# Kernel optimization log

Hardware: AMD Instinct MI355X
Metric: run time of the kernel (lower is better)

## Reference

```python
import jax, jax.numpy as jnp
import numpy as np

KNOTS = 17
T_MAX = 3.0


def _trapezoid(knots=KNOTS, t_max=T_MAX):
    t = jnp.linspace(0.0, t_max, knots, dtype=jnp.float32)
    dt = t_max / (knots - 1)
    w = jnp.full((knots,), 2.0 * dt, dtype=jnp.float32)
    w = w.at[0].set(dt).at[-1].set(dt)
    weights = w * jnp.exp(-t * t / 2.0)
    return t, weights


def setup_inputs() -> dict:
    key = jax.random.key(0)
    k1, k2 = jax.random.split(key)
    z = jax.random.normal(k1, (32, 128, 512), dtype=jnp.float32)   # (T, B, D)
    A = jax.random.normal(k2, (512, 1024), dtype=jnp.float32)      # (D, M) raw, normalized inside
    return {"z": z, "A": A}


def reference(z, A):
    t, weights = _trapezoid()                       # (K,), (K,)
    # column-normalize random projections (matches A / A.norm(dim=0).clamp_min(1e-12))
    norm = jnp.sqrt(jnp.sum(A * A, axis=0, keepdims=True))
    An = A / jnp.maximum(norm, 1e-12)
    proj = jnp.einsum('tbd,dm->tbm', z, An)         # (T, B, M)
    xt = proj[..., None] * t                        # (T, B, M, K) — dominant intermediate
    cos_mean = jnp.mean(jnp.cos(xt), axis=1)        # reduce over B -> (T, M, K)
    sin_mean = jnp.mean(jnp.sin(xt), axis=1)
    target = jnp.exp(-t * t / 2.0)                  # (K,)
    err = (cos_mean - target) ** 2 + sin_mean ** 2  # (T, M, K)
    statistic = err @ weights                       # (T, M)
    statistic = statistic * z.shape[1]              # multiply by B (proj.size(-2))
    return jnp.mean(statistic)
```

## Files before the change

### kernel.cpp

```cpp
#include <hip/hip_runtime.h>
#include <hip/hip_bf16.h>
#include <math.h>

#define T_DIM 32
#define B_DIM 128
#define D_DIM 512
#define M_DIM 1024

constexpr float DT = 0.1875f;
constexpr float INV_2PI = 0.15915494309189535f;

typedef __attribute__((ext_vector_type(8))) short bf16x8;
typedef __attribute__((ext_vector_type(4))) float f32x4;
typedef __attribute__((ext_vector_type(2))) float f32x2;

__device__ __forceinline__ ushort f2bf(float f) {
    unsigned u = __float_as_uint(f);
    u += 0x7FFFu + ((u >> 16) & 1u);
    return (ushort)(u >> 16);
}

__device__ __forceinline__ void gload16(const void* g, void* l) {
    __builtin_amdgcn_global_load_lds(
        (const __attribute__((address_space(1))) void*)g,
        (__attribute__((address_space(3))) void*)l, 16, 0, 0);
}

__device__ __forceinline__ void fast_sincos(float theta, float& s, float& c) {
    float r = theta * INV_2PI;
    r -= floorf(r);
    s = __builtin_amdgcn_sinf(r);
    c = __builtin_amdgcn_cosf(r);
}

__global__ __launch_bounds__(256) void prep_kernel(const float* __restrict__ A,
                                                   const float* __restrict__ z,
                                                   ushort* __restrict__ zb,
                                                   ushort* __restrict__ ant) {
    const int bid = blockIdx.x;
    const int tid = threadIdx.x;

    if (bid >= 64) {
        const size_t base = (size_t)(bid - 64) * 4096 + tid * 8;
#pragma unroll
        for (int j = 0; j < 2; ++j) {
            const size_t i = base + j * 2048;
            const float4 a = *reinterpret_cast<const float4*>(&z[i]);
            const float4 b = *reinterpret_cast<const float4*>(&z[i + 4]);
            uint4 p;
            p.x = (unsigned)f2bf(a.x) | ((unsigned)f2bf(a.y) << 16);
            p.y = (unsigned)f2bf(a.z) | ((unsigned)f2bf(a.w) << 16);
            p.z = (unsigned)f2bf(b.x) | ((unsigned)f2bf(b.y) << 16);
            p.w = (unsigned)f2bf(b.z) | ((unsigned)f2bf(b.w) << 16);
            *reinterpret_cast<uint4*>(&zb[i]) = p;
        }
        return;
    }

    __shared__ float red[256];
    __shared__ float inv[16];
    __shared__ float tile[128][17];

    const int mB = bid * 16;
    const int mo = tid & 15;
    const int dg = tid >> 4;
    float ss = 0.0f;
#pragma unroll 4
    for (int i = 0; i < 32; ++i) {
        const float v = A[(size_t)(dg * 32 + i) * M_DIM + mB + mo];
        ss = fmaf(v, v, ss);
    }
    red[tid] = ss;
    __syncthreads();
    for (int s = 128; s >= 16; s >>= 1) {
        if (tid < s) red[tid] += red[tid + s];
        __syncthreads();
    }
    if (tid < 16) inv[tid] = 1.0f / fmaxf(sqrtf(red[tid]), 1e-12f);

#pragma unroll
    for (int ch = 0; ch < 4; ++ch) {
        const int dB = ch * 128;
#pragma unroll
        for (int q = 0; q < 2; ++q) {
            const int s  = tid + 256 * q;
            const int r  = s >> 2;
            const int c4 = (s & 3) * 4;
            const float4 v = *reinterpret_cast<const float4*>(
                &A[(size_t)(dB + r) * M_DIM + mB + c4]);
            tile[r][c4]     = v.x;
            tile[r][c4 + 1] = v.y;
            tile[r][c4 + 2] = v.z;
            tile[r][c4 + 3] = v.w;
        }
        __syncthreads();
        {
            const int m  = tid >> 4;
            const int d8 = (tid & 15) * 8;
            const float sc = inv[m];
            uint4 p;
            p.x = (unsigned)f2bf(tile[d8 + 0][m] * sc) | ((unsigned)f2bf(tile[d8 + 1][m] * sc) << 16);
            p.y = (unsigned)f2bf(tile[d8 + 2][m] * sc) | ((unsigned)f2bf(tile[d8 + 3][m] * sc) << 16);
            p.z = (unsigned)f2bf(tile[d8 + 4][m] * sc) | ((unsigned)f2bf(tile[d8 + 5][m] * sc) << 16);
            p.w = (unsigned)f2bf(tile[d8 + 6][m] * sc) | ((unsigned)f2bf(tile[d8 + 7][m] * sc) << 16);
            *reinterpret_cast<uint4*>(&ant[(size_t)(mB + m) * D_DIM + dB + d8]) = p;
        }
        __syncthreads();
    }
}

#define CHEB(CS) { const f32x2 nxt = c2 * cur - prev; prev = cur; cur = nxt; CS += cur; }
#define CF_ALL(V) { \
    float s1, c1; fast_sincos((V) * DT, s1, c1); \
    const float c2 = 2.0f * c1; \
    f32x2 prev = {1.0f, 0.0f}; \
    f32x2 cur  = {c1, s1}; \
    cs0 += cur; \
    CHEB(cs1)  CHEB(cs2)  CHEB(cs3)  CHEB(cs4)  CHEB(cs5) \
    CHEB(cs6)  CHEB(cs7)  CHEB(cs8)  CHEB(cs9)  CHEB(cs10) \
    CHEB(cs11) CHEB(cs12) CHEB(cs13) CHEB(cs14) CHEB(cs15) }
#define RED(CS) { \
    CS.x += __shfl_xor(CS.x, 16); CS.x += __shfl_xor(CS.x, 32); \
    CS.y += __shfl_xor(CS.y, 16); CS.y += __shfl_xor(CS.y, 32); }
#define ST(CS, K) { wred[wc][l15][K] = CS.x; wred[wc][l15][16 + K] = CS.y; }
#define FIN(CS, KK) { \
    constexpr float tk = DT * (float)(KK); \
    const float g  = __expf(-0.5f * tk * tk); \
    const float w  = (((KK) == 16) ? DT : 2.0f * DT) * g; \
    const float totC = wred[wc][l15][(KK) - 1]      + CS.x; \
    const float totS = wred[wc][l15][16 + (KK) - 1] + CS.y; \
    const float cm = fmaf(totC, invB, -g); \
    const float sm = totS * invB; \
    s = fmaf(w, fmaf(cm, cm, sm * sm), s); }

__global__ __launch_bounds__(512) void fused_kernel(const ushort* __restrict__ zb,
                                                    const ushort* __restrict__ ant,
                                                    float* __restrict__ partials) {
    __shared__ __align__(16) union SharedU {
        ushort As[128 * 128];
        struct { float wred[4][16][33]; float bred[4]; } r;
    } u;
    __shared__ __align__(16) ushort Bs[64 * 128];

    const int tid  = threadIdx.x;
    const int bid  = blockIdx.x;
    const int idx  = bid >> 3;
    const int t    = (bid & 7) * 4 + (idx & 3);
    const int mBi  = idx >> 2;
    const int mB   = mBi * 64;

    const int wave = tid >> 6;
    const int lane = tid & 63;
    const int wr   = wave >> 2;
    const int wc   = wave & 3;
    const int l15  = lane & 15;
    const int lhi  = lane >> 4;

    const int rofs = lane >> 4;
    const int gl   = lane & 15;

    const ushort* zrow = zb + (size_t)t * B_DIM * D_DIM;

    f32x4 acc[4];
#pragma unroll
    for (int fm = 0; fm < 4; ++fm) acc[fm] = (f32x4)(0.0f);

#pragma unroll
    for (int it = 0; it < 4; ++it) {
        const int k0 = it * 128;
#pragma unroll
        for (int j = 0; j < 4; ++j) {
            const int r0  = wave * 16 + j * 4;
            const int row = r0 + rofs;
            const int gs  = gl ^ (row & 15);
            gload16(&zrow[(size_t)row * D_DIM + k0 + gs * 8], &u.As[r0 * 128]);
        }
#pragma unroll
        for (int j = 0; j < 2; ++j) {
            const int r0  = wave * 8 + j * 4;
            const int row = r0 + rofs;
            const int gs  = gl ^ (row & 15);
            gload16(&ant[(size_t)(mB + row) * D_DIM + k0 + gs * 8], &Bs[r0 * 128]);
        }
        __syncthreads();

#pragma unroll
        for (int ks = 0; ks < 4; ++ks) {
            const int gd = (ks * 4 + lhi) ^ l15;
            const int co = gd * 8;
            const bf16x8 bfrag = *reinterpret_cast<const bf16x8*>(&Bs[(wc * 16 + l15) * 128 + co]);
#pragma unroll
            for (int fm = 0; fm < 4; ++fm) {
                const bf16x8 afrag = *reinterpret_cast<const bf16x8*>(&u.As[(wr * 64 + fm * 16 + l15) * 128 + co]);
                acc[fm] = __builtin_amdgcn_mfma_f32_16x16x32_bf16(afrag, bfrag, acc[fm], 0, 0, 0);
            }
        }
        __syncthreads();
    }

    float (&wred)[4][16][33] = u.r.wred;
    float (&bred)[4] = u.r.bred;

    f32x2 cs0  = {0.f, 0.f}, cs1  = {0.f, 0.f}, cs2  = {0.f, 0.f}, cs3  = {0.f, 0.f};
    f32x2 cs4  = {0.f, 0.f}, cs5  = {0.f, 0.f}, cs6  = {0.f, 0.f}, cs7  = {0.f, 0.f};
    f32x2 cs8  = {0.f, 0.f}, cs9  = {0.f, 0.f}, cs10 = {0.f, 0.f}, cs11 = {0.f, 0.f};
    f32x2 cs12 = {0.f, 0.f}, cs13 = {0.f, 0.f}, cs14 = {0.f, 0.f}, cs15 = {0.f, 0.f};

#pragma unroll
    for (int fm = 0; fm < 4; ++fm) {
        const f32x4 av = acc[fm];
        CF_ALL(av.x) CF_ALL(av.y) CF_ALL(av.z) CF_ALL(av.w)
    }

    RED(cs0)  RED(cs1)  RED(cs2)  RED(cs3)  RED(cs4)  RED(cs5)  RED(cs6)  RED(cs7)
    RED(cs8)  RED(cs9)  RED(cs10) RED(cs11) RED(cs12) RED(cs13) RED(cs14) RED(cs15)

    if (wr == 0 && lane < 16) {
        ST(cs0, 0)   ST(cs1, 1)   ST(cs2, 2)   ST(cs3, 3)
        ST(cs4, 4)   ST(cs5, 5)   ST(cs6, 6)   ST(cs7, 7)
        ST(cs8, 8)   ST(cs9, 9)   ST(cs10, 10) ST(cs11, 11)
        ST(cs12, 12) ST(cs13, 13) ST(cs14, 14) ST(cs15, 15)
    }
    __syncthreads();

    float s = 0.0f;
    if (wr == 1) {
        const float invB = 1.0f / 128.0f;
        FIN(cs0, 1)   FIN(cs1, 2)   FIN(cs2, 3)   FIN(cs3, 4)
        FIN(cs4, 5)   FIN(cs5, 6)   FIN(cs6, 7)   FIN(cs7, 8)
        FIN(cs8, 9)   FIN(cs9, 10)  FIN(cs10, 11) FIN(cs11, 12)
        FIN(cs12, 13) FIN(cs13, 14) FIN(cs14, 15) FIN(cs15, 16)
#pragma unroll
        for (int m = 1; m < 64; m <<= 1) s += __shfl_xor(s, m);
        if (lane == 0) bred[wc] = s;
    }
    __syncthreads();
    if (tid == 0)
        partials[t * 16 + mBi] = bred[0] + bred[1] + bred[2] + bred[3];
}

__global__ __launch_bounds__(256) void finalize_kernel(const float* __restrict__ partials,
                                                       float* __restrict__ out) {
    __shared__ float red[256];
    const int tid = threadIdx.x;
    red[tid] = partials[tid] + partials[tid + 256];
    __syncthreads();
    for (int s = 128; s > 0; s >>= 1) {
        if (tid < s) red[tid] += red[tid + s];
        __syncthreads();
    }
    if (tid == 0) out[0] = red[0] * (1.0f / 1024.0f);
}

extern "C" void kernel_launch(void* const* d_in, const int* in_sizes, int n_in,
                              void* d_out, int out_size, void* d_ws, size_t ws_size,
                              hipStream_t stream) {
    const float* z = (const float*)d_in[0];
    const float* A = (const float*)d_in[1];
    float* out = (float*)d_out;

    char* ws = (char*)d_ws;
    ushort* zb       = (ushort*)ws;
    ushort* ant      = (ushort*)(ws + 4 * 1024 * 1024);
    float*  partials = (float*)(ws + 5 * 1024 * 1024);

    prep_kernel<<<576, 256, 0, stream>>>(A, z, zb, ant);
    fused_kernel<<<512, 512, 0, stream>>>(zb, ant, partials);
    finalize_kernel<<<1, 256, 0, stream>>>(partials, out);
}
```

Measured before the change: 26.74 us.

## Switch fused GEMM to 32x32x16 MFMA with 128-wide M tiles

```diff
diff --git a/kernel.cpp b/kernel.cpp
--- a/kernel.cpp
+++ b/kernel.cpp
@@ -10,9 +10,9 @@
 constexpr float DT = 0.1875f;
 constexpr float INV_2PI = 0.15915494309189535f;
 
-typedef __attribute__((ext_vector_type(8))) short bf16x8;
-typedef __attribute__((ext_vector_type(4))) float f32x4;
-typedef __attribute__((ext_vector_type(2))) float f32x2;
+typedef __attribute__((ext_vector_type(8)))  short bf16x8;
+typedef __attribute__((ext_vector_type(16))) float f32x16;
+typedef __attribute__((ext_vector_type(2)))  float f32x2;
 
 __device__ __forceinline__ ushort f2bf(float f) {
     unsigned u = __float_as_uint(f);
@@ -119,16 +119,14 @@
     CHEB(cs1)  CHEB(cs2)  CHEB(cs3)  CHEB(cs4)  CHEB(cs5) \
     CHEB(cs6)  CHEB(cs7)  CHEB(cs8)  CHEB(cs9)  CHEB(cs10) \
     CHEB(cs11) CHEB(cs12) CHEB(cs13) CHEB(cs14) CHEB(cs15) }
-#define RED(CS) { \
-    CS.x += __shfl_xor(CS.x, 16); CS.x += __shfl_xor(CS.x, 32); \
-    CS.y += __shfl_xor(CS.y, 16); CS.y += __shfl_xor(CS.y, 32); }
-#define ST(CS, K) { wred[wc][l15][K] = CS.x; wred[wc][l15][16 + K] = CS.y; }
+#define RED32(CS) { CS.x += __shfl_xor(CS.x, 32); CS.y += __shfl_xor(CS.y, 32); }
+#define ST(CS, K) { wred[wc][l31][K] = CS.x; wred[wc][l31][16 + K] = CS.y; }
 #define FIN(CS, KK) { \
     constexpr float tk = DT * (float)(KK); \
     const float g  = __expf(-0.5f * tk * tk); \
     const float w  = (((KK) == 16) ? DT : 2.0f * DT) * g; \
-    const float totC = wred[wc][l15][(KK) - 1]      + CS.x; \
-    const float totS = wred[wc][l15][16 + (KK) - 1] + CS.y; \
+    const float totC = wred[wc][l31][(KK) - 1]      + CS.x; \
+    const float totS = wred[wc][l31][16 + (KK) - 1] + CS.y; \
     const float cm = fmaf(totC, invB, -g); \
     const float sm = totS * invB; \
     s = fmaf(w, fmaf(cm, cm, sm * sm), s); }
@@ -138,32 +136,32 @@
                                                     float* __restrict__ partials) {
     __shared__ __align__(16) union SharedU {
         ushort As[128 * 128];
-        struct { float wred[4][16][33]; float bred[4]; } r;
+        struct { float wred[4][32][33]; float bred[4]; } r;
     } u;
-    __shared__ __align__(16) ushort Bs[64 * 128];
-
-    const int tid  = threadIdx.x;
+    __shared__ __align__(16) ushort Bs[128 * 128];
+
+    const int tid = threadIdx.x;
     const int bid  = blockIdx.x;
     const int idx  = bid >> 3;
     const int t    = (bid & 7) * 4 + (idx & 3);
     const int mBi  = idx >> 2;
-    const int mB   = mBi * 64;
+    const int mB   = mBi * 128;
 
     const int wave = tid >> 6;
     const int lane = tid & 63;
     const int wr   = wave >> 2;
     const int wc   = wave & 3;
-    const int l15  = lane & 15;
-    const int lhi  = lane >> 4;
+    const int l31  = lane & 31;
+    const int lh5  = lane >> 5;
 
     const int rofs = lane >> 4;
     const int gl   = lane & 15;
 
     const ushort* zrow = zb + (size_t)t * B_DIM * D_DIM;
 
-    f32x4 acc[4];
-#pragma unroll
-    for (int fm = 0; fm < 4; ++fm) acc[fm] = (f32x4)(0.0f);
+    f32x16 acc[2];
+    acc[0] = (f32x16)(0.0f);
+    acc[1] = (f32x16)(0.0f);
 
 #pragma unroll
     for (int it = 0; it < 4; ++it) {
@@ -176,8 +174,8 @@
             gload16(&zrow[(size_t)row * D_DIM + k0 + gs * 8], &u.As[r0 * 128]);
         }
 #pragma unroll
-        for (int j = 0; j < 2; ++j) {
-            const int r0  = wave * 8 + j * 4;
+        for (int j = 0; j < 4; ++j) {
+            const int r0  = wave * 16 + j * 4;
             const int row = r0 + rofs;
             const int gs  = gl ^ (row & 15);
             gload16(&ant[(size_t)(mB + row) * D_DIM + k0 + gs * 8], &Bs[r0 * 128]);
@@ -185,20 +183,22 @@
         __syncthreads();
 
 #pragma unroll
-        for (int ks = 0; ks < 4; ++ks) {
-            const int gd = (ks * 4 + lhi) ^ l15;
-            const int co = gd * 8;
-            const bf16x8 bfrag = *reinterpret_cast<const bf16x8*>(&Bs[(wc * 16 + l15) * 128 + co]);
-#pragma unroll
-            for (int fm = 0; fm < 4; ++fm) {
-                const bf16x8 afrag = *reinterpret_cast<const bf16x8*>(&u.As[(wr * 64 + fm * 16 + l15) * 128 + co]);
-                acc[fm] = __builtin_amdgcn_mfma_f32_16x16x32_bf16(afrag, bfrag, acc[fm], 0, 0, 0);
+        for (int ks = 0; ks < 8; ++ks) {
+            const int brow = wc * 32 + l31;
+            const int bco  = ((ks * 2 + lh5) ^ (brow & 15)) * 8;
+            const bf16x8 bfrag = *reinterpret_cast<const bf16x8*>(&Bs[brow * 128 + bco]);
+#pragma unroll
+            for (int bt = 0; bt < 2; ++bt) {
+                const int arow = wr * 64 + bt * 32 + l31;
+                const int aco  = ((ks * 2 + lh5) ^ (arow & 15)) * 8;
+                const bf16x8 afrag = *reinterpret_cast<const bf16x8*>(&u.As[arow * 128 + aco]);
+                acc[bt] = __builtin_amdgcn_mfma_f32_32x32x16_bf16(afrag, bfrag, acc[bt], 0, 0, 0);
             }
         }
         __syncthreads();
     }
 
-    float (&wred)[4][16][33] = u.r.wred;
+    float (&wred)[4][32][33] = u.r.wred;
     float (&bred)[4] = u.r.bred;
 
     f32x2 cs0  = {0.f, 0.f}, cs1  = {0.f, 0.f}, cs2  = {0.f, 0.f}, cs3  = {0.f, 0.f};
@@ -207,15 +207,20 @@
     f32x2 cs12 = {0.f, 0.f}, cs13 = {0.f, 0.f}, cs14 = {0.f, 0.f}, cs15 = {0.f, 0.f};
 
 #pragma unroll
-    for (int fm = 0; fm < 4; ++fm) {
-        const f32x4 av = acc[fm];
-        CF_ALL(av.x) CF_ALL(av.y) CF_ALL(av.z) CF_ALL(av.w)
-    }
-
-    RED(cs0)  RED(cs1)  RED(cs2)  RED(cs3)  RED(cs4)  RED(cs5)  RED(cs6)  RED(cs7)
-    RED(cs8)  RED(cs9)  RED(cs10) RED(cs11) RED(cs12) RED(cs13) RED(cs14) RED(cs15)
-
-    if (wr == 0 && lane < 16) {
+    for (int bt = 0; bt < 2; ++bt) {
+        const f32x16 av = acc[bt];
+#pragma unroll
+        for (int r = 0; r < 16; ++r) {
+            CF_ALL(av[r])
+        }
+    }
+
+    RED32(cs0)  RED32(cs1)  RED32(cs2)  RED32(cs3)
+    RED32(cs4)  RED32(cs5)  RED32(cs6)  RED32(cs7)
+    RED32(cs8)  RED32(cs9)  RED32(cs10) RED32(cs11)
+    RED32(cs12) RED32(cs13) RED32(cs14) RED32(cs15)
+
+    if (wr == 0 && lane < 32) {
         ST(cs0, 0)   ST(cs1, 1)   ST(cs2, 2)   ST(cs3, 3)
         ST(cs4, 4)   ST(cs5, 5)   ST(cs6, 6)   ST(cs7, 7)
         ST(cs8, 8)   ST(cs9, 9)   ST(cs10, 10) ST(cs11, 11)
@@ -236,20 +241,20 @@
     }
     __syncthreads();
     if (tid == 0)
-        partials[t * 16 + mBi] = bred[0] + bred[1] + bred[2] + bred[3];
+        partials[t * 8 + mBi] = bred[0] + bred[1] + bred[2] + bred[3];
 }
 
 __global__ __launch_bounds__(256) void finalize_kernel(const float* __restrict__ partials,
                                                        float* __restrict__ out) {
     __shared__ float red[256];
     const int tid = threadIdx.x;
-    red[tid] = partials[tid] + partials[tid + 256];
+    red[tid] = partials[tid];
     __syncthreads();
     for (int s = 128; s > 0; s >>= 1) {
         if (tid < s) red[tid] += red[tid + s];
         __syncthreads();
     }
-    if (tid == 0) out[0] = red[0] * (1.0f / 1024.0f);
+    if (tid == 0) out[0] = red[0] * (1.0f / 512.0f);
 }
 
 extern "C" void kernel_launch(void* const* d_in, const int* in_sizes, int n_in,
@@ -265,6 +270,6 @@
     float*  partials = (float*)(ws + 5 * 1024 * 1024);
 
     prep_kernel<<<576, 256, 0, stream>>>(A, z, zb, ant);
-    fused_kernel<<<512, 512, 0, stream>>>(zb, ant, partials);
+    fused_kernel<<<256, 512, 0, stream>>>(zb, ant, partials);
     finalize_kernel<<<1, 256, 0, stream>>>(partials, out);
 }
```

Measured after the change: 26.98 us. About the same (+0.9%).
